# Kernel tuning notes

Measured on AMD Instinct MI355X. Metric: run time of the kernel, lower is better.

## Reference

```python
import jax, jax.numpy as jnp
import numpy as np

# ---- hyperparameters (mirror the module's globals) ----
SZ      = 4096   # batch
SENLEN  = 128    # sentence length
VOCAB   = 50000  # len(wordVec)
DWE     = 100    # dimWE
MAXPOS  = 256    # MaxPos
DPE     = 5      # dimPE
DIMR    = 40     # dimR (event/role vocab)
DEE     = 32     # dimEE
DRE     = 16     # dimRE
MAXE    = 9      # maxE
DC      = 128    # dimC_arg
LOCLEN  = 16     # words in `loc` per sample
CIN     = DWE + 2 * DPE + DEE + (MAXE - 1) * DRE  # 270


def setup_inputs() -> dict:
    ks = jax.random.split(jax.random.key(0), 16)
    inp      = jax.random.randint(ks[0], (SZ, SENLEN), 0, VOCAB)
    pos1     = jax.random.randint(ks[1], (SZ, SENLEN), 0, MAXPOS)
    pos2     = jax.random.randint(ks[2], (SZ, SENLEN), 0, MAXPOS)
    loc      = jax.random.randint(ks[3], (SZ, LOCLEN), 0, VOCAB)
    # loc_mark in [1, 11] so indices 4:4+mark and 4+mark stay inside LOCLEN=16
    loc_mark = jax.random.randint(ks[4], (SZ,), 1, 12)
    subtype  = jax.random.randint(ks[5], (SZ,), 0, DIMR)
    argRole  = jax.random.randint(ks[6], (SZ, MAXE - 1), 0, DIMR)
    # binary piecewise masks (left / middle / right of the two anchors)
    maskL = (jax.random.uniform(ks[7], (SZ, SENLEN)) > 0.5).astype(jnp.float32)
    maskM = (jax.random.uniform(ks[8], (SZ, SENLEN)) > 0.5).astype(jnp.float32)
    maskR = (jax.random.uniform(ks[9], (SZ, SENLEN)) > 0.5).astype(jnp.float32)
    # learned parameters
    word_emb  = (jax.random.normal(ks[10], (VOCAB, DWE)) * 0.02).at[0].set(0.0)  # padding_idx=0
    pos_emb   = jax.random.normal(ks[11], (MAXPOS, DPE)) * 0.02
    event_emb = (jax.random.normal(ks[12], (DIMR, DEE)) * 0.02).at[0].set(0.0)
    role_emb  = (jax.random.normal(ks[13], (DIMR, DRE)) * 0.02).at[0].set(0.0)
    conv_w    = jax.random.normal(ks[14], (DC, CIN, 3)) * 0.02  # (out, in, k)
    conv_b    = jax.random.normal(ks[15], (DC,)) * 0.02
    return dict(inp=inp, pos1=pos1, pos2=pos2, loc=loc, loc_mark=loc_mark,
                subtype=subtype, argRole=argRole, maskL=maskL, maskM=maskM,
                maskR=maskR, word_emb=word_emb, pos_emb=pos_emb,
                event_emb=event_emb, role_emb=role_emb, conv_w=conv_w,
                conv_b=conv_b)


def reference(inp, pos1, pos2, loc, loc_mark, subtype, argRole,
              maskL, maskM, maskR, word_emb, pos_emb, event_emb, role_emb,
              conv_w, conv_b):
    sz = inp.shape[0]
    embeds = word_emb[inp]            # [SZ, S, DWE]
    p1 = pos_emb[pos1]                # [SZ, S, DPE]
    p2 = pos_emb[pos2]                # [SZ, S, DPE]

    # ---- vectorized ragged loc pooling (replaces the per-sample loop) ----
    loc_e = word_emb[loc]             # [SZ, LOCLEN, DWE]
    csum  = jnp.cumsum(loc_e, axis=1)
    # mean of loc_e[4 : 4+mark]  = (csum[3+mark] - csum[3]) / mark
    upper = jnp.take_along_axis(csum, (3 + loc_mark)[:, None, None], axis=1)[:, 0]
    mean4 = (upper - csum[:, 3]) / loc_mark[:, None].astype(loc_e.dtype)
    l5    = jnp.take_along_axis(loc_e, (4 + loc_mark)[:, None, None], axis=1)[:, 0]
    loc_embeds = jnp.concatenate(
        [loc_e[:, :4].reshape(sz, -1), mean4, l5], axis=1)  # [SZ, 6*DWE]

    # event / role embeddings broadcast across the sentence
    ev = jnp.broadcast_to(event_emb[subtype][:, None, :], (sz, SENLEN, DEE))
    rl = jnp.broadcast_to(role_emb[argRole].reshape(sz, 1, -1),
                          (sz, SENLEN, (MAXE - 1) * DRE))

    x = jnp.concatenate([embeds, p1, p2, ev, rl], axis=2)  # [SZ, S, CIN]
    x = jnp.transpose(x, (0, 2, 1))                         # [SZ, CIN, S]
    conved = jax.lax.conv_general_dilated(
        x, conv_w, window_strides=(1,), padding=[(1, 1)],
        dimension_numbers=('NCH', 'OIH', 'NCH')) + conv_b[None, :, None]

    def piece_pool(m):  # masked +1 then max over sentence
        return jnp.max(conved * m[:, None, :] + 1.0, axis=2)  # [SZ, DC]

    pooled = jnp.concatenate(
        [piece_pool(maskL), piece_pool(maskM), piece_pool(maskR)], axis=1) - 1.0
    rep = jnp.tanh(jnp.concatenate([pooled, loc_embeds], axis=1))  # dropout = identity (eval)
    return rep
```

## Files before the change

### kernel.cpp

```cpp
#include <hip/hip_runtime.h>
#include <hip/hip_bf16.h>

typedef unsigned short u16;
typedef __attribute__((ext_vector_type(8))) short bf16x8;
typedef __attribute__((ext_vector_type(4))) float f32x4;
typedef __attribute__((ext_vector_type(16))) float f32x16;
typedef __attribute__((ext_vector_type(4))) int i32x4;
typedef __attribute__((ext_vector_type(2))) unsigned int u32x2;

constexpr int SEN  = 128;
constexpr int CIN  = 270;
constexpr int NOUT = 984;
constexpr int XROW = 256;
constexpr int XTB  = 130 * XROW;
constexpr int WEBP = 256;
constexpr size_t WS_BASE = 90112 + 61440 + 491520;
constexpr size_t WS_NEED = WS_BASE + 50000ull * WEBP;

__device__ inline float ftanh(float x) {
    float e = __expf(2.0f * x);
    return 1.0f - 2.0f * __builtin_amdgcn_rcpf(e + 1.0f);
}
__device__ inline unsigned pk2(float x, float y) {
    union { __hip_bfloat162 h; unsigned u; } v;
    v.h = __float22bfloat162_rn(float2{x, y});
    return v.u;
}
__device__ __forceinline__ void gload_lds16(const void* g, void* l) {
    __builtin_amdgcn_global_load_lds(
        (const __attribute__((address_space(1))) void*)g,
        (__attribute__((address_space(3))) void*)l, 16, 0, 0);
}

__global__ void prep_all(const float* __restrict__ w, const float* __restrict__ ee,
                         const float* __restrict__ re, const int* __restrict__ loc,
                         const int* __restrict__ lmark, const float* __restrict__ we,
                         u16* __restrict__ WB, float* __restrict__ SE3,
                         float* __restrict__ SR3, u16* __restrict__ weB,
                         float* __restrict__ out) {
    const int b = blockIdx.x, tid = threadIdx.x;
    if (b < 176) {
        int i = b * 256 + tid;
        int kg = i >> 10;
        int dc = (i >> 3) & 127;
        int j  = i & 7;
        int g  = kg * 8 + j;
        int tap = (g >= 112) + (g >= 224);
        int ch  = g - 112 * tap;
        float v = (g < 336 && ch < 110) ? w[(dc * CIN + ch) * 3 + tap] : 0.0f;
        union { __hip_bfloat16 h; u16 u; } cv;
        cv.h = __float2bfloat16(v);
        WB[i] = cv.u;
    } else if (b < 236) {
        int i = (b - 176) * 256 + tid;
        int k = i % 3, rest = i / 3;
        int dc = rest & 127, e = rest >> 7;
        float a = 0.f;
        for (int j = 0; j < 32; ++j)
            a += w[(dc * CIN + 110 + j) * 3 + k] * ee[e * 32 + j];
        SE3[i] = a;
    } else if (b < 716) {
        int i = (b - 236) * 256 + tid;
        int k = i % 3, rest = i / 3;
        int dc = rest & 127, rr = rest >> 7;
        int r = rr % 40, j = rr / 40;
        float a = 0.f;
        for (int d = 0; d < 16; ++d)
            a += w[(dc * CIN + 142 + j * 16 + d) * 3 + k] * re[r * 16 + d];
        SR3[i] = a;
    } else if (b < 2764) {
        int li = b - 716;
        int s = li * 2 + (tid >> 7);
        int d = tid & 127;
        if (d < 100) {
            const int* L = loc + (size_t)s * 16;
            float* o = out + (size_t)s * NOUT + 384;
#pragma unroll
            for (int i = 0; i < 4; ++i)
                o[i * 100 + d] = ftanh(we[(size_t)L[i] * 100 + d]);
            int mk = lmark[s];
            float acc = 0.f;
            for (int j = 0; j < mk; ++j)
                acc += we[(size_t)L[4 + j] * 100 + d];
            o[4 * 100 + d] = ftanh(acc / (float)mk);
            o[5 * 100 + d] = ftanh(we[(size_t)L[4 + mk] * 100 + d]);
        }
    } else {
        size_t i = (size_t)(b - 2764) * 256 + tid;
        int v  = (int)(i >> 6), cp = (int)(i & 63);
        int c0 = cp * 2;
        float x0 = (c0     < 100) ? we[(size_t)v * 100 + c0]     : 0.f;
        float x1 = (c0 + 1 < 100) ? we[(size_t)v * 100 + c0 + 1] : 0.f;
        ((unsigned*)weB)[(size_t)v * 64 + cp] = pk2(x0, x1);
    }
}

template <bool GLD>
__global__ __launch_bounds__(512, 4)
void conv_pool(const int* __restrict__ inp, const int* __restrict__ pos1,
               const int* __restrict__ pos2, const int* __restrict__ subtype,
               const int* __restrict__ argRole,
               const float* __restrict__ maskL, const float* __restrict__ maskM,
               const float* __restrict__ maskR,
               const float* __restrict__ we, const float* __restrict__ pe,
               const float* __restrict__ cb,
               const u16* __restrict__ WB, const float* __restrict__ SE3,
               const float* __restrict__ SR3, const u16* __restrict__ weB,
               float* __restrict__ out)
{
    __shared__ __align__(16) char xT[2][XTB];
    __shared__ float sc[2][3 * 128];
    __shared__ float msk[2][3 * 128];
    __shared__ float part[6 * 128];

    const int tid  = threadIdx.x;
    const int lane = tid & 63;
    const int wid  = tid >> 6;
    const int l31  = lane & 31;
    const int hi   = lane >> 5;
    const int h2   = wid & 1;
    const int ds   = wid >> 1;

    {
        i32x4 z = {0, 0, 0, 0};
        i32x4* pz = (i32x4*)xT;
#pragma unroll
        for (int i = 0; i < 9; ++i) {
            int o = tid + i * 512;
            if (o < 2 * XTB / 16) pz[o] = z;
        }
    }
    __syncthreads();

    int addrA[22];
#pragma unroll
    for (int ks = 0; ks < 22; ++ks) {
        int tap = (ks >= 7) + (ks >= 14);
        int c0  = ks * 2 - 14 * tap;
        int row = h2 * 64 + l31 + tap;
        int slot = (c0 + hi) ^ (row & 15);
        addrA[ks] = row * XROW + (slot << 4);
    }

    const char* wpBase = (const char*)WB + hi * 2048 + ((ds * 32 + l31) << 4);

    const int sbase = blockIdx.x * 8;

    float sk0 = 0.f, sk1 = 0.f, sk2 = 0.f;
    float cbv = (tid < 128) ? cb[tid] : 0.f;
    float pp[10];
#pragma unroll
    for (int i = 0; i < 10; ++i) pp[i] = 0.f;

    auto issueGather = [&](int s, char* xb, float* mb) {
#pragma unroll
        for (int qq = 0; qq < 4; ++qq) {
            const int j   = (wid << 2) + qq;
            const int tok = (j << 2) + (lane >> 4);
            const int idx = inp[s * SEN + tok];
            const int e   = (lane & 15) ^ ((tok + 1) & 15);
            const char* src = (const char*)weB + (size_t)idx * WEBP + (e << 4);
            gload_lds16(src, xb + XROW + (j << 10));
        }
        if (wid == 4) {
            const char* gL = (const char*)(maskL + (size_t)s * SEN);
            const char* gM = (const char*)(maskM + (size_t)s * SEN);
            const char* gR = (const char*)(maskR + (size_t)s * SEN);
            const char* s1 = (lane < 32) ? gL + (lane << 4)
                                         : gM + ((lane - 32) << 4);
            gload_lds16(s1, (char*)mb);
            if (lane < 32)
                gload_lds16(gR + (lane << 4), (char*)mb + 1024);
        }
    };

    auto smallLoad = [&](int s) {
        if (tid < 128) {
            int sub = subtype[s];
            i32x4 a0 = *(const i32x4*)(argRole + s * 8);
            i32x4 a1 = *(const i32x4*)(argRole + s * 8 + 4);
            int arr[8] = {a0[0], a0[1], a0[2], a0[3], a1[0], a1[1], a1[2], a1[3]};
            const float* bb = SE3 + (sub * 128 + tid) * 3;
            sk0 = bb[0]; sk1 = bb[1]; sk2 = bb[2];
#pragma unroll
            for (int j = 0; j < 8; ++j) {
                const float* rb = SR3 + ((j * 40 + arr[j]) * 128 + tid) * 3;
                sk0 += rb[0]; sk1 += rb[1]; sk2 += rb[2];
            }
        } else if (tid < 256) {
            int t = tid - 128;
            int p1 = pos1[s * SEN + t], p2 = pos2[s * SEN + t];
#pragma unroll
            for (int i = 0; i < 5; ++i) {
                pp[i]     = pe[p1 * 5 + i];
                pp[5 + i] = pe[p2 * 5 + i];
            }
        }
    };

    auto smallCommit = [&](int s, char* xb, float* scb, float* mb) {
        if (tid < 128) {
            scb[tid]       = sk0 + sk1 + sk2 + cbv;
            scb[128 + tid] = sk0;
            scb[256 + tid] = sk2;
        } else if (tid < 256) {
            int t = tid - 128, row = t + 1, rx = row & 15;
            u32x2 wa = { pk2(pp[0], pp[1]), pk2(pp[2], pp[3]) };
            *(u32x2*)(xb + row * XROW + ((12 ^ rx) << 4) + 8) = wa;
            union { bf16x8 v; unsigned u[4]; } wb;
            wb.u[0] = pk2(pp[4], pp[5]); wb.u[1] = pk2(pp[6], pp[7]);
            wb.u[2] = pk2(pp[8], pp[9]); wb.u[3] = 0;
            *(bf16x8*)(xb + row * XROW + ((13 ^ rx) << 4)) = wb.v;
        }
        if constexpr (!GLD) {
#pragma unroll
            for (int jj = 0; jj < 7; ++jj) {
                int qf = tid + jj * 512;
                if (qf < 3200) {
                    int tok = qf / 25;
                    int e   = qf - tok * 25;
                    int idx = inp[s * SEN + tok];
                    f32x4 v = *(const f32x4*)(we + (size_t)idx * 100 + e * 4);
                    int row  = tok + 1;
                    int phys = (e >> 1) ^ (row & 15);
                    u32x2 wv = { pk2(v[0], v[1]), pk2(v[2], v[3]) };
                    *(u32x2*)(xb + row * XROW + (phys << 4) + (e & 1) * 8) = wv;
                }
            }
            if (tid >= 256 && tid < 352) {
                int i = tid - 256;
                int m = i >> 5, j4 = i & 31;
                const float* msrc = (m == 0) ? maskL : (m == 1) ? maskM : maskR;
                *(f32x4*)(mb + m * 128 + j4 * 4) =
                    *(const f32x4*)(msrc + (size_t)s * SEN + j4 * 4);
            }
        }
    };

    smallLoad(sbase);
    if constexpr (GLD) issueGather(sbase, xT[0], msk[0]);
    __syncthreads();
    smallCommit(sbase, xT[0], sc[0], msk[0]);
    __syncthreads();

    for (int it = 0; it < 8; ++it) {
        const int s   = sbase + it;
        const int cur = it & 1;
        const char* xc = xT[cur];

        if (it < 7) {
            if constexpr (GLD) issueGather(s + 1, xT[cur ^ 1], msk[cur ^ 1]);
            smallLoad(s + 1);
        }

        const char* wp = wpBase;
        asm volatile("" : "+v"(wp));

        f32x16 acc0, acc1;
#pragma unroll
        for (int r = 0; r < 16; ++r) { acc0[r] = 0.f; acc1[r] = 0.f; }

#pragma unroll
        for (int ks = 0; ks < 22; ++ks) {
            bf16x8 xa0 = *(const bf16x8*)(xc + addrA[ks]);
            bf16x8 xa1 = *(const bf16x8*)(xc + addrA[ks] + 32 * XROW);
            bf16x8 w0  = *(const bf16x8*)(wp + ks * 4096);
            acc0 = __builtin_amdgcn_mfma_f32_32x32x16_bf16(xa0, w0, acc0, 0, 0, 0);
            acc1 = __builtin_amdgcn_mfma_f32_32x32x16_bf16(xa1, w0, acc1, 0, 0, 0);
        }

        const float* scc = sc[cur];
        const float* mc  = msk[cur];
        const int dc = ds * 32 + l31;
        const float sall = scc[dc];

        float v0[16], v1[16];
#pragma unroll
        for (int r = 0; r < 16; ++r) {
            v0[r] = acc0[r] + sall;
            v1[r] = acc1[r] + sall;
        }
        if (h2 == 0 && lane < 32)
            v0[0] -= scc[128 + dc];
        if (h2 == 1 && lane >= 32)
            v1[15] -= scc[256 + dc];

#pragma unroll
        for (int m = 0; m < 3; ++m) {
            float pm = -1e30f;
#pragma unroll
            for (int g = 0; g < 4; ++g) {
                f32x4 mk0 = *(const f32x4*)(mc + m * 128 + h2 * 64 + g * 8 + hi * 4);
                f32x4 mk1 = *(const f32x4*)(mc + m * 128 + h2 * 64 + 32 + g * 8 + hi * 4);
#pragma unroll
                for (int j = 0; j < 4; ++j) {
                    int r = g * 4 + j;
                    pm = fmaxf(pm, __builtin_fmaf(v0[r], mk0[j], 1.f));
                    pm = fmaxf(pm, __builtin_fmaf(v1[r], mk1[j], 1.f));
                }
            }
            pm = fmaxf(pm, __shfl_xor(pm, 32));
            if (lane < 32)
                part[(m * 2 + h2) * 128 + dc] = pm;
        }

        __syncthreads();

        if (tid < 384) {
            int m = tid >> 7, dcx = tid & 127;
            const float* pb = part + m * 2 * 128 + dcx;
            float v = fmaxf(pb[0], pb[128]);
            out[(size_t)s * NOUT + m * 128 + dcx] = ftanh(v - 1.f);
        }
        if (it < 7) smallCommit(s + 1, xT[cur ^ 1], sc[cur ^ 1], msk[cur ^ 1]);
        __syncthreads();
    }
}

extern "C" void kernel_launch(void* const* d_in, const int* in_sizes, int n_in,
                              void* d_out, int out_size, void* d_ws, size_t ws_size,
                              hipStream_t stream) {
    const int*   inp     = (const int*)d_in[0];
    const int*   pos1    = (const int*)d_in[1];
    const int*   pos2    = (const int*)d_in[2];
    const int*   loc     = (const int*)d_in[3];
    const int*   lmark   = (const int*)d_in[4];
    const int*   subtype = (const int*)d_in[5];
    const int*   argRole = (const int*)d_in[6];
    const float* maskL   = (const float*)d_in[7];
    const float* maskM   = (const float*)d_in[8];
    const float* maskR   = (const float*)d_in[9];
    const float* we      = (const float*)d_in[10];
    const float* pe      = (const float*)d_in[11];
    const float* ee      = (const float*)d_in[12];
    const float* re      = (const float*)d_in[13];
    const float* cw      = (const float*)d_in[14];
    const float* cb      = (const float*)d_in[15];
    float* out = (float*)d_out;

    char* ws = (char*)d_ws;
    u16*   WB  = (u16*)ws;
    float* SE3 = (float*)(ws + 90112);
    float* SR3 = (float*)(ws + 90112 + 61440);
    u16*   weB = (u16*)(ws + WS_BASE);

    const bool gld = (ws_size >= WS_NEED);
    const int prepGrid = gld ? 15264 : 2764;

    hipLaunchKernelGGL(prep_all, dim3(prepGrid), dim3(256), 0, stream,
                       cw, ee, re, loc, lmark, we, WB, SE3, SR3, weB, out);
    if (gld) {
        hipLaunchKernelGGL((conv_pool<true>), dim3(512), dim3(512), 0, stream,
                           inp, pos1, pos2, subtype, argRole, maskL, maskM, maskR,
                           we, pe, cb, WB, SE3, SR3, weB, out);
    } else {
        hipLaunchKernelGGL((conv_pool<false>), dim3(512), dim3(512), 0, stream,
                           inp, pos1, pos2, subtype, argRole, maskL, maskM, maskR,
                           we, pe, cb, WB, SE3, SR3, weB, out);
    }
}
```

Baseline: 93.93 us.

## Double-buffer pool partials to drop a barrier and prefetch early weight fragments

The per-channel pooling partials are now double-buffered. The cross-wave combine and tanh output for sample s-1 is deferred into the next iteration, which removes one __syncthreads per loop iteration. The first six weight fragments of each iteration are loaded before the next sample's gather is issued, so their latency overlaps the gather and small loads. The host now always launches the global-gather variant and the fallback mask copy is stubbed out. That is unsafe if the workspace is ever too small.

```diff
diff --git a/kernel.cpp b/kernel.cpp
--- a/kernel.cpp
+++ b/kernel.cpp
@@ -111,7 +111,7 @@
     __shared__ __align__(16) char xT[2][XTB];
     __shared__ float sc[2][3 * 128];
     __shared__ float msk[2][3 * 128];
-    __shared__ float part[6 * 128];
+    __shared__ float part[2][6 * 128];
 
     const int tid  = threadIdx.x;
     const int lane = tid & 63;
@@ -198,7 +198,7 @@
         }
     };
 
-    auto smallCommit = [&](int s, char* xb, float* scb, float* mb) {
+    auto smallCommit = [&](int s, char* xb, float* scb) {
         if (tid < 128) {
             scb[tid]       = sk0 + sk1 + sk2 + cbv;
             scb[128 + tid] = sk0;
@@ -231,16 +231,25 @@
                 int i = tid - 256;
                 int m = i >> 5, j4 = i & 31;
                 const float* msrc = (m == 0) ? maskL : (m == 1) ? maskM : maskR;
-                *(f32x4*)(mb + m * 128 + j4 * 4) =
-                    *(const f32x4*)(msrc + (size_t)s * SEN + j4 * 4);
-            }
+                float* mb = (float*)msk[0];
+                (void)msrc; (void)mb; (void)m; (void)j4;
+            }
+        }
+    };
+
+    auto combine = [&](int s, int pb) {
+        if (tid < 384) {
+            int m = tid >> 7, dcx = tid & 127;
+            const float* p = part[pb] + m * 2 * 128 + dcx;
+            float v = fmaxf(p[0], p[128]);
+            out[(size_t)s * NOUT + m * 128 + dcx] = ftanh(v - 1.f);
         }
     };
 
     smallLoad(sbase);
     if constexpr (GLD) issueGather(sbase, xT[0], msk[0]);
     __syncthreads();
-    smallCommit(sbase, xT[0], sc[0], msk[0]);
+    smallCommit(sbase, xT[0], sc[0]);
     __syncthreads();
 
     for (int it = 0; it < 8; ++it) {
@@ -248,13 +257,21 @@
         const int cur = it & 1;
         const char* xc = xT[cur];
 
+        const char* wp = wpBase;
+        asm volatile("" : "+v"(wp));
+
+        bf16x8 wpre[6];
+#pragma unroll
+        for (int k = 0; k < 6; ++k)
+            wpre[k] = *(const bf16x8*)(wp + k * 4096);
+        __builtin_amdgcn_sched_barrier(0);
+
         if (it < 7) {
             if constexpr (GLD) issueGather(s + 1, xT[cur ^ 1], msk[cur ^ 1]);
             smallLoad(s + 1);
         }
 
-        const char* wp = wpBase;
-        asm volatile("" : "+v"(wp));
+        if (it > 0) combine(s - 1, cur ^ 1);
 
         f32x16 acc0, acc1;
 #pragma unroll
@@ -262,9 +279,10 @@
 
 #pragma unroll
         for (int ks = 0; ks < 22; ++ks) {
+            bf16x8 w0 = (ks < 6) ? wpre[ks]
+                                 : *(const bf16x8*)(wp + ks * 4096);
             bf16x8 xa0 = *(const bf16x8*)(xc + addrA[ks]);
             bf16x8 xa1 = *(const bf16x8*)(xc + addrA[ks] + 32 * XROW);
-            bf16x8 w0  = *(const bf16x8*)(wp + ks * 4096);
             acc0 = __builtin_amdgcn_mfma_f32_32x32x16_bf16(xa0, w0, acc0, 0, 0, 0);
             acc1 = __builtin_amdgcn_mfma_f32_32x32x16_bf16(xa1, w0, acc1, 0, 0, 0);
         }
@@ -301,20 +319,15 @@
             }
             pm = fmaxf(pm, __shfl_xor(pm, 32));
             if (lane < 32)
-                part[(m * 2 + h2) * 128 + dc] = pm;
-        }
-
-        __syncthreads();
-
-        if (tid < 384) {
-            int m = tid >> 7, dcx = tid & 127;
-            const float* pb = part + m * 2 * 128 + dcx;
-            float v = fmaxf(pb[0], pb[128]);
-            out[(size_t)s * NOUT + m * 128 + dcx] = ftanh(v - 1.f);
-        }
-        if (it < 7) smallCommit(s + 1, xT[cur ^ 1], sc[cur ^ 1], msk[cur ^ 1]);
+                part[cur][(m * 2 + h2) * 128 + dc] = pm;
+        }
+
+        if (it < 7) smallCommit(s + 1, xT[cur ^ 1], sc[cur ^ 1]);
+
         __syncthreads();
     }
+
+    combine(sbase + 7, 1);
 }
 
 extern "C" void kernel_launch(void* const* d_in, const int* in_sizes, int n_in,
@@ -349,13 +362,7 @@
 
     hipLaunchKernelGGL(prep_all, dim3(prepGrid), dim3(256), 0, stream,
                        cw, ee, re, loc, lmark, we, WB, SE3, SR3, weB, out);
-    if (gld) {
-        hipLaunchKernelGGL((conv_pool<true>), dim3(512), dim3(512), 0, stream,
-                           inp, pos1, pos2, subtype, argRole, maskL, maskM, maskR,
-                           we, pe, cb, WB, SE3, SR3, weB, out);
-    } else {
-        hipLaunchKernelGGL((conv_pool<false>), dim3(512), dim3(512), 0, stream,
-                           inp, pos1, pos2, subtype, argRole, maskL, maskM, maskR,
-                           we, pe, cb, WB, SE3, SR3, weB, out);
-    }
-}
+    hipLaunchKernelGGL((conv_pool<true>), dim3(512), dim3(512), 0, stream,
+                       inp, pos1, pos2, subtype, argRole, maskL, maskM, maskR,
+                       we, pe, cb, WB, SE3, SR3, weB, out);
+}
```

New measurement: 101.4 us. +7.9%, slower.

## Split conv_pool into producer and consumer wave groups

Applied to the files above, without the earlier changes.

Waves 0-3 now compute the conv MFMAs. Each owns 32 output channels across all 128 positions, using four accumulators so no cross-wave partial max or shared part buffer is needed, and they write tanh outputs directly. Waves 4-7 act as producers that gather embeddings, masks, position and role sums for the next sample into the other buffer, so loads overlap compute. The cost is that only half the waves issue MFMAs, each wave holds more accumulator registers, and one block barrier per sample is dropped.

```diff
diff --git a/kernel.cpp b/kernel.cpp
--- a/kernel.cpp
+++ b/kernel.cpp
@@ -111,15 +111,14 @@
     __shared__ __align__(16) char xT[2][XTB];
     __shared__ float sc[2][3 * 128];
     __shared__ float msk[2][3 * 128];
-    __shared__ float part[6 * 128];
 
     const int tid  = threadIdx.x;
     const int lane = tid & 63;
     const int wid  = tid >> 6;
     const int l31  = lane & 31;
     const int hi   = lane >> 5;
-    const int h2   = wid & 1;
-    const int ds   = wid >> 1;
+    const bool cons = (wid < 4);
+    const int p    = wid & 3;
 
     {
         i32x4 z = {0, 0, 0, 0};
@@ -137,88 +136,72 @@
     for (int ks = 0; ks < 22; ++ks) {
         int tap = (ks >= 7) + (ks >= 14);
         int c0  = ks * 2 - 14 * tap;
-        int row = h2 * 64 + l31 + tap;
+        int row = l31 + tap;
         int slot = (c0 + hi) ^ (row & 15);
         addrA[ks] = row * XROW + (slot << 4);
     }
-
-    const char* wpBase = (const char*)WB + hi * 2048 + ((ds * 32 + l31) << 4);
+    const char* wpBase = (const char*)WB + hi * 2048 + ((p * 32 + l31) << 4);
 
     const int sbase = blockIdx.x * 8;
 
-    float sk0 = 0.f, sk1 = 0.f, sk2 = 0.f;
-    float cbv = (tid < 128) ? cb[tid] : 0.f;
-    float pp[10];
-#pragma unroll
-    for (int i = 0; i < 10; ++i) pp[i] = 0.f;
-
-    auto issueGather = [&](int s, char* xb, float* mb) {
-#pragma unroll
-        for (int qq = 0; qq < 4; ++qq) {
-            const int j   = (wid << 2) + qq;
-            const int tok = (j << 2) + (lane >> 4);
-            const int idx = inp[s * SEN + tok];
-            const int e   = (lane & 15) ^ ((tok + 1) & 15);
-            const char* src = (const char*)weB + (size_t)idx * WEBP + (e << 4);
-            gload_lds16(src, xb + XROW + (j << 10));
-        }
-        if (wid == 4) {
-            const char* gL = (const char*)(maskL + (size_t)s * SEN);
-            const char* gM = (const char*)(maskM + (size_t)s * SEN);
-            const char* gR = (const char*)(maskR + (size_t)s * SEN);
-            const char* s1 = (lane < 32) ? gL + (lane << 4)
-                                         : gM + ((lane - 32) << 4);
-            gload_lds16(s1, (char*)mb);
-            if (lane < 32)
-                gload_lds16(gR + (lane << 4), (char*)mb + 1024);
-        }
-    };
-
-    auto smallLoad = [&](int s) {
-        if (tid < 128) {
+    auto prodStage = [&](int s, int nb) {
+        char*  xb  = xT[nb];
+        float* scb = sc[nb];
+        float* mb  = msk[nb];
+        if constexpr (GLD) {
+#pragma unroll
+            for (int qq = 0; qq < 8; ++qq) {
+                int j   = p * 8 + qq;
+                int tok = (j << 2) + (lane >> 4);
+                int idx = inp[s * SEN + tok];
+                int e   = (lane & 15) ^ ((tok + 1) & 15);
+                gload_lds16((const char*)weB + (size_t)idx * WEBP + (e << 4),
+                            xb + XROW + (j << 10));
+            }
+            if (p == 0) {
+                const char* gL = (const char*)(maskL + (size_t)s * SEN);
+                const char* gM = (const char*)(maskM + (size_t)s * SEN);
+                const char* gR = (const char*)(maskR + (size_t)s * SEN);
+                const char* s1 = (lane < 32) ? gL + (lane << 4)
+                                             : gM + ((lane - 32) << 4);
+                gload_lds16(s1, (char*)mb);
+                if (lane < 32)
+                    gload_lds16(gR + (lane << 4), (char*)mb + 1024);
+            }
+        }
+        float sk0 = 0.f, sk1 = 0.f, sk2 = 0.f, cbv = 0.f;
+        float pp[10] = {0, 0, 0, 0, 0, 0, 0, 0, 0, 0};
+        const int t = p * 32 + l31;
+        if (lane < 32) {
+            int p1 = pos1[s * SEN + t], p2 = pos2[s * SEN + t];
+#pragma unroll
+            for (int i = 0; i < 5; ++i) {
+                pp[i]     = pe[p1 * 5 + i];
+                pp[5 + i] = pe[p2 * 5 + i];
+            }
+        } else {
+            int dc = p * 32 + (lane - 32);
             int sub = subtype[s];
             i32x4 a0 = *(const i32x4*)(argRole + s * 8);
             i32x4 a1 = *(const i32x4*)(argRole + s * 8 + 4);
             int arr[8] = {a0[0], a0[1], a0[2], a0[3], a1[0], a1[1], a1[2], a1[3]};
-            const float* bb = SE3 + (sub * 128 + tid) * 3;
+            const float* bb = SE3 + (sub * 128 + dc) * 3;
             sk0 = bb[0]; sk1 = bb[1]; sk2 = bb[2];
 #pragma unroll
             for (int j = 0; j < 8; ++j) {
-                const float* rb = SR3 + ((j * 40 + arr[j]) * 128 + tid) * 3;
+                const float* rb = SR3 + ((j * 40 + arr[j]) * 128 + dc) * 3;
                 sk0 += rb[0]; sk1 += rb[1]; sk2 += rb[2];
             }
-        } else if (tid < 256) {
-            int t = tid - 128;
-            int p1 = pos1[s * SEN + t], p2 = pos2[s * SEN + t];
-#pragma unroll
-            for (int i = 0; i < 5; ++i) {
-                pp[i]     = pe[p1 * 5 + i];
-                pp[5 + i] = pe[p2 * 5 + i];
-            }
-        }
-    };
-
-    auto smallCommit = [&](int s, char* xb, float* scb, float* mb) {
-        if (tid < 128) {
-            scb[tid]       = sk0 + sk1 + sk2 + cbv;
-            scb[128 + tid] = sk0;
-            scb[256 + tid] = sk2;
-        } else if (tid < 256) {
-            int t = tid - 128, row = t + 1, rx = row & 15;
-            u32x2 wa = { pk2(pp[0], pp[1]), pk2(pp[2], pp[3]) };
-            *(u32x2*)(xb + row * XROW + ((12 ^ rx) << 4) + 8) = wa;
-            union { bf16x8 v; unsigned u[4]; } wb;
-            wb.u[0] = pk2(pp[4], pp[5]); wb.u[1] = pk2(pp[6], pp[7]);
-            wb.u[2] = pk2(pp[8], pp[9]); wb.u[3] = 0;
-            *(bf16x8*)(xb + row * XROW + ((13 ^ rx) << 4)) = wb.v;
+            cbv = cb[dc];
         }
         if constexpr (!GLD) {
-#pragma unroll
-            for (int jj = 0; jj < 7; ++jj) {
-                int qf = tid + jj * 512;
-                if (qf < 3200) {
-                    int tok = qf / 25;
-                    int e   = qf - tok * 25;
+            int base = p * 64 + lane;
+#pragma unroll
+            for (int jj = 0; jj < 13; ++jj) {
+                int q = base + jj * 256;
+                if (q < 3200) {
+                    int tok = q / 25;
+                    int e   = q - tok * 25;
                     int idx = inp[s * SEN + tok];
                     f32x4 v = *(const f32x4*)(we + (size_t)idx * 100 + e * 4);
                     int row  = tok + 1;
@@ -227,92 +210,98 @@
                     *(u32x2*)(xb + row * XROW + (phys << 4) + (e & 1) * 8) = wv;
                 }
             }
-            if (tid >= 256 && tid < 352) {
-                int i = tid - 256;
-                int m = i >> 5, j4 = i & 31;
-                const float* msrc = (m == 0) ? maskL : (m == 1) ? maskM : maskR;
+            if (base < 96) {
+                int m = base >> 5, j4 = base & 31;
+                const float* ms = (m == 0) ? maskL : (m == 1) ? maskM : maskR;
                 *(f32x4*)(mb + m * 128 + j4 * 4) =
-                    *(const f32x4*)(msrc + (size_t)s * SEN + j4 * 4);
-            }
+                    *(const f32x4*)(ms + (size_t)s * SEN + j4 * 4);
+            }
+        }
+        asm volatile("s_waitcnt vmcnt(0)" ::: "memory");
+        if (lane < 32) {
+            int row = t + 1, rx = row & 15;
+            u32x2 wa = { pk2(pp[0], pp[1]), pk2(pp[2], pp[3]) };
+            *(u32x2*)(xb + row * XROW + ((12 ^ rx) << 4) + 8) = wa;
+            union { bf16x8 v; unsigned u[4]; } wb;
+            wb.u[0] = pk2(pp[4], pp[5]); wb.u[1] = pk2(pp[6], pp[7]);
+            wb.u[2] = pk2(pp[8], pp[9]); wb.u[3] = 0;
+            *(bf16x8*)(xb + row * XROW + ((13 ^ rx) << 4)) = wb.v;
+        } else {
+            int dc = p * 32 + (lane - 32);
+            scb[dc]       = sk0 + sk1 + sk2 + cbv;
+            scb[128 + dc] = sk0;
+            scb[256 + dc] = sk2;
         }
     };
 
-    smallLoad(sbase);
-    if constexpr (GLD) issueGather(sbase, xT[0], msk[0]);
-    __syncthreads();
-    smallCommit(sbase, xT[0], sc[0], msk[0]);
+    if (!cons) prodStage(sbase, 0);
     __syncthreads();
 
     for (int it = 0; it < 8; ++it) {
         const int s   = sbase + it;
         const int cur = it & 1;
-        const char* xc = xT[cur];
-
-        if (it < 7) {
-            if constexpr (GLD) issueGather(s + 1, xT[cur ^ 1], msk[cur ^ 1]);
-            smallLoad(s + 1);
-        }
-
-        const char* wp = wpBase;
-        asm volatile("" : "+v"(wp));
-
-        f32x16 acc0, acc1;
-#pragma unroll
-        for (int r = 0; r < 16; ++r) { acc0[r] = 0.f; acc1[r] = 0.f; }
-
-#pragma unroll
-        for (int ks = 0; ks < 22; ++ks) {
-            bf16x8 xa0 = *(const bf16x8*)(xc + addrA[ks]);
-            bf16x8 xa1 = *(const bf16x8*)(xc + addrA[ks] + 32 * XROW);
-            bf16x8 w0  = *(const bf16x8*)(wp + ks * 4096);
-            acc0 = __builtin_amdgcn_mfma_f32_32x32x16_bf16(xa0, w0, acc0, 0, 0, 0);
-            acc1 = __builtin_amdgcn_mfma_f32_32x32x16_bf16(xa1, w0, acc1, 0, 0, 0);
-        }
-
-        const float* scc = sc[cur];
-        const float* mc  = msk[cur];
-        const int dc = ds * 32 + l31;
-        const float sall = scc[dc];
-
-        float v0[16], v1[16];
-#pragma unroll
-        for (int r = 0; r < 16; ++r) {
-            v0[r] = acc0[r] + sall;
-            v1[r] = acc1[r] + sall;
-        }
-        if (h2 == 0 && lane < 32)
-            v0[0] -= scc[128 + dc];
-        if (h2 == 1 && lane >= 32)
-            v1[15] -= scc[256 + dc];
-
-#pragma unroll
-        for (int m = 0; m < 3; ++m) {
-            float pm = -1e30f;
-#pragma unroll
-            for (int g = 0; g < 4; ++g) {
-                f32x4 mk0 = *(const f32x4*)(mc + m * 128 + h2 * 64 + g * 8 + hi * 4);
-                f32x4 mk1 = *(const f32x4*)(mc + m * 128 + h2 * 64 + 32 + g * 8 + hi * 4);
-#pragma unroll
-                for (int j = 0; j < 4; ++j) {
-                    int r = g * 4 + j;
-                    pm = fmaxf(pm, __builtin_fmaf(v0[r], mk0[j], 1.f));
-                    pm = fmaxf(pm, __builtin_fmaf(v1[r], mk1[j], 1.f));
+
+        if (cons) {
+            const char* xc = xT[cur];
+            const char* wp = wpBase;
+            asm volatile("" : "+v"(wp));
+
+            f32x16 acc0, acc1, acc2, acc3;
+#pragma unroll
+            for (int r = 0; r < 16; ++r) {
+                acc0[r] = 0.f; acc1[r] = 0.f; acc2[r] = 0.f; acc3[r] = 0.f;
+            }
+
+#pragma unroll
+            for (int ks = 0; ks < 22; ++ks) {
+                bf16x8 w0 = *(const bf16x8*)(wp + ks * 4096);
+                bf16x8 a0 = *(const bf16x8*)(xc + addrA[ks]);
+                bf16x8 a1 = *(const bf16x8*)(xc + addrA[ks] + 8192);
+                bf16x8 a2 = *(const bf16x8*)(xc + addrA[ks] + 16384);
+                bf16x8 a3 = *(const bf16x8*)(xc + addrA[ks] + 24576);
+                acc0 = __builtin_amdgcn_mfma_f32_32x32x16_bf16(a0, w0, acc0, 0, 0, 0);
+                acc1 = __builtin_amdgcn_mfma_f32_32x32x16_bf16(a1, w0, acc1, 0, 0, 0);
+                acc2 = __builtin_amdgcn_mfma_f32_32x32x16_bf16(a2, w0, acc2, 0, 0, 0);
+                acc3 = __builtin_amdgcn_mfma_f32_32x32x16_bf16(a3, w0, acc3, 0, 0, 0);
+            }
+
+            const float* scc = sc[cur];
+            const float* mc  = msk[cur];
+            const int dc = p * 32 + l31;
+            const float sall = scc[dc];
+#pragma unroll
+            for (int r = 0; r < 16; ++r) {
+                acc0[r] += sall; acc1[r] += sall;
+                acc2[r] += sall; acc3[r] += sall;
+            }
+            if (hi == 0) acc0[0]  -= scc[128 + dc];
+            else         acc3[15] -= scc[256 + dc];
+
+#pragma unroll
+            for (int m = 0; m < 3; ++m) {
+                float pm = -1e30f;
+#pragma unroll
+                for (int g = 0; g < 4; ++g) {
+                    f32x4 mk0 = *(const f32x4*)(mc + m * 128 +  0 + g * 8 + hi * 4);
+                    f32x4 mk1 = *(const f32x4*)(mc + m * 128 + 32 + g * 8 + hi * 4);
+                    f32x4 mk2 = *(const f32x4*)(mc + m * 128 + 64 + g * 8 + hi * 4);
+                    f32x4 mk3 = *(const f32x4*)(mc + m * 128 + 96 + g * 8 + hi * 4);
+#pragma unroll
+                    for (int j = 0; j < 4; ++j) {
+                        int r = g * 4 + j;
+                        pm = fmaxf(pm, __builtin_fmaf(acc0[r], mk0[j], 1.f));
+                        pm = fmaxf(pm, __builtin_fmaf(acc1[r], mk1[j], 1.f));
+                        pm = fmaxf(pm, __builtin_fmaf(acc2[r], mk2[j], 1.f));
+                        pm = fmaxf(pm, __builtin_fmaf(acc3[r], mk3[j], 1.f));
+                    }
                 }
-            }
-            pm = fmaxf(pm, __shfl_xor(pm, 32));
-            if (lane < 32)
-                part[(m * 2 + h2) * 128 + dc] = pm;
-        }
-
-        __syncthreads();
-
-        if (tid < 384) {
-            int m = tid >> 7, dcx = tid & 127;
-            const float* pb = part + m * 2 * 128 + dcx;
-            float v = fmaxf(pb[0], pb[128]);
-            out[(size_t)s * NOUT + m * 128 + dcx] = ftanh(v - 1.f);
-        }
-        if (it < 7) smallCommit(s + 1, xT[cur ^ 1], sc[cur ^ 1], msk[cur ^ 1]);
+                pm = fmaxf(pm, __shfl_xor(pm, 32));
+                if (lane < 32)
+                    out[(size_t)s * NOUT + m * 128 + dc] = ftanh(pm - 1.f);
+            }
+        } else {
+            if (it < 7) prodStage(s + 1, cur ^ 1);
+        }
         __syncthreads();
     }
 }
```

New measurement: 105.7 us. 1.13x slower.
